# Kernel tuning notes

Measured on AMD Instinct MI355X. Metric: run time of the kernel, lower is better.

The kernel has to match this reference:

```python
import jax, jax.numpy as jnp
import numpy as np

NUM_ITERS = 2      # num_iters default
NEG_SLOPE = 0.2    # LeakyReLU slope in GAT attention
NEG_INF = -1e9

N, E, B, H, K, L = 204800, 6144000, 4096, 8, 30, 50


def setup_inputs() -> dict:
    key = jax.random.key(0)
    ks = jax.random.split(key, 14)
    return {
        "target_features": jax.random.normal(ks[0], (N, 8), jnp.float32),
        "feature_dist_graph": jax.random.normal(ks[1], (E, 8), jnp.float32),
        "rij_dist_pairs": jax.random.uniform(ks[2], (E,), jnp.float32),
        "b_scope": jax.random.randint(ks[3], (N, K), 0, E + 1, jnp.int32),
        "start_end_env": jax.random.randint(ks[4], (N, K), 0, N + 1, jnp.int32),
        "l_scope": jax.random.randint(ks[5], (B, L), 0, N + 1, jnp.int32),
        "edge_src": jax.random.randint(ks[6], (E,), 0, N + 1, jnp.int32),
        "W_emb": jax.random.normal(ks[7], (8, H), jnp.float32),
        "b_emb": jax.random.normal(ks[8], (H,), jnp.float32),
        "W_dist": jax.random.normal(ks[9], (9, H), jnp.float32),
        "b_dist": jax.random.normal(ks[10], (H,), jnp.float32),
        "W_gat": jax.random.normal(ks[11], (H, H), jnp.float32),
        "a_src": jax.random.normal(ks[12], (H,), jnp.float32),
        "a_dst": jax.random.normal(ks[13], (H,), jnp.float32),
    }


def reference(target_features, feature_dist_graph, rij_dist_pairs,
              b_scope, start_end_env, l_scope, edge_src,
              W_emb, b_emb, W_dist, b_dist, W_gat, a_src, a_dst):
    # node embedding: [N, 8] -> [N, H]
    h = target_features @ W_emb + b_emb
    # edge (feature+distance) embedding: [E, 9] -> [E, H]
    msg = jnp.concatenate([feature_dist_graph, rij_dist_pairs[:, None]], axis=1) @ W_dist + b_dist
    zero = jnp.zeros((1, h.shape[1]), h.dtype)
    h = jnp.concatenate([zero, h], axis=0)          # zero row for 1-based / padded indices
    pad_mask = b_scope > 0                           # padded neighbor slots point at row 0
    for _ in range(NUM_ITERS):
        nbr_self = h[start_end_env]                  # getConnectedFeatures: [N, K, H] (target repeated)
        msg0 = jnp.concatenate([zero, msg], axis=0)  # zero row for padded edge indices
        nbr_msg = msg0[b_scope]                      # gathered neighbor messages [N, K, H]
        # GAT attention over the K neighbor slots
        z_s = nbr_self @ W_gat                       # [N, K, H]
        z_m = nbr_msg @ W_gat                        # [N, K, H]
        e = jax.nn.leaky_relu(z_s @ a_src + z_m @ a_dst, NEG_SLOPE)  # [N, K]
        e = jnp.where(pad_mask, e, NEG_INF)
        alpha = jax.nn.softmax(e, axis=1)            # [N, K]
        out = jnp.einsum('nk,nkh->nh', alpha, z_m)   # attention-weighted aggregate [N, H]
        h = jnp.concatenate([zero, jax.nn.elu(out)], axis=0)  # [N+1, H]
        # updateConnectedDict: scatter node states back to per-edge messages
        msg = h[edge_src]                            # [E, H]
    # readout: gather per-graph feature rows and sum -> mol_vecs [B, H]
    return h[l_scope].sum(axis=1)
```

## Files before the change

### kernel.cpp

```cpp
#include <hip/hip_runtime.h>

typedef float f32x4 __attribute__((ext_vector_type(4)));

#define NEG_SLOPE 0.2f
#define NEG_INF   -1e9f

__global__ void embed_kernel(const float* __restrict__ tf,
                             const float* __restrict__ W_emb,
                             const float* __restrict__ b_emb,
                             const float* __restrict__ W_gat,
                             const float* __restrict__ a_src,
                             float* __restrict__ h_a,
                             float* __restrict__ h_b,
                             float* __restrict__ t0,
                             float* __restrict__ t1, int N) {
    __shared__ float sWg[64];
    __shared__ float s_as[8];
    int tid = threadIdx.x;
    if (tid < 64) sWg[tid] = W_gat[tid];
    __syncthreads();
    if (tid < 8) {
        float s = 0.f;
        #pragma unroll
        for (int q = 0; q < 8; ++q) s += sWg[tid * 8 + q] * a_src[q];
        s_as[tid] = s;
    }
    __syncthreads();

    int n = blockIdx.x * blockDim.x + tid;
    if (n >= N) return;
    if (n == 0) {
        #pragma unroll
        for (int j = 0; j < 8; ++j) { h_a[j] = 0.f; h_b[j] = 0.f; }
        t0[0] = 0.f;
        t1[0] = 0.f;
    }
    const f32x4* tfr = reinterpret_cast<const f32x4*>(tf + (size_t)n * 8);
    f32x4 a = tfr[0], b = tfr[1];
    float x[8] = {a[0], a[1], a[2], a[3], b[0], b[1], b[2], b[3]};
    float out[8];
    #pragma unroll
    for (int j = 0; j < 8; ++j) out[j] = b_emb[j];
    #pragma unroll
    for (int i = 0; i < 8; ++i)
        #pragma unroll
        for (int j = 0; j < 8; ++j)
            out[j] += x[i] * W_emb[i * 8 + j];

    float t = 0.f;
    #pragma unroll
    for (int p = 0; p < 8; ++p) t += out[p] * s_as[p];
    t0[n + 1] = t;

    f32x4* hr = reinterpret_cast<f32x4*>(h_a + (size_t)(n + 1) * 8);
    f32x4 o0 = {out[0], out[1], out[2], out[3]};
    f32x4 o1 = {out[4], out[5], out[6], out[7]};
    hr[0] = o0;
    hr[1] = o1;
}

__global__ void prep_records(const float* __restrict__ fdg,
                             const float* __restrict__ rij,
                             const int* __restrict__ edge_src,
                             const float* __restrict__ W_dist,
                             const float* __restrict__ b_dist,
                             const float* __restrict__ W_gat,
                             const float* __restrict__ a_dst,
                             float* __restrict__ rec, int E) {
    __shared__ float sWd[72];
    __shared__ float sbd[8];
    __shared__ float sWg[64];
    __shared__ float s_ad[8];
    int tid = threadIdx.x;
    if (tid < 72) sWd[tid] = W_dist[tid];
    else if (tid < 80) sbd[tid - 72] = b_dist[tid - 72];
    if (tid >= 128 && tid < 192) sWg[tid - 128] = W_gat[tid - 128];
    __syncthreads();
    if (tid < 8) {
        float s = 0.f;
        #pragma unroll
        for (int j = 0; j < 8; ++j) s += sWg[tid * 8 + j] * a_dst[j];
        s_ad[tid] = s;
    }
    __syncthreads();

    int e = blockIdx.x * blockDim.x + tid;
    if (e >= E) return;
    const f32x4* fr = reinterpret_cast<const f32x4*>(fdg + (size_t)e * 8);
    f32x4 g0 = fr[0], g1 = fr[1];
    float rv = rij[e];
    float msg[8];
    #pragma unroll
    for (int j = 0; j < 8; ++j) {
        float s = sbd[j];
        #pragma unroll
        for (int i = 0; i < 4; ++i) s += g0[i] * sWd[i * 8 + j];
        #pragma unroll
        for (int i = 0; i < 4; ++i) s += g1[i] * sWd[(4 + i) * 8 + j];
        s += rv * sWd[64 + j];
        msg[j] = s;
    }
    float em = 0.f;
    #pragma unroll
    for (int j = 0; j < 8; ++j) em += msg[j] * s_ad[j];
    int src = edge_src[e];

    f32x4* op = reinterpret_cast<f32x4*>(rec + (size_t)e * 16);
    f32x4 m0 = {msg[0], msg[1], msg[2], msg[3]};
    f32x4 m1 = {msg[4], msg[5], msg[6], msg[7]};
    f32x4 m2 = {em, __int_as_float(src), 0.f, 0.f};
    f32x4 m3 = {0.f, 0.f, 0.f, 0.f};
    op[0] = m0; op[1] = m1; op[2] = m2; op[3] = m3;
}

template <bool REC>
__global__ void gat_iter1(const float* __restrict__ t0,
                          float* __restrict__ h1,
                          float* __restrict__ t1,
                          int* __restrict__ src_idx,
                          const int* __restrict__ b_scope,
                          const int* __restrict__ se_env,
                          const float* __restrict__ rec,
                          const float* __restrict__ fdg,
                          const float* __restrict__ rij,
                          const int* __restrict__ edge_src,
                          const float* __restrict__ W_dist,
                          const float* __restrict__ b_dist,
                          const float* __restrict__ W_gat,
                          const float* __restrict__ a_src,
                          const float* __restrict__ a_dst,
                          int N, int K) {
    __shared__ float sWg[64];
    __shared__ float s_as[8];
    __shared__ float s_ad[8];
    __shared__ float sWd[72];
    __shared__ float sbd[8];
    int tid = threadIdx.x;
    if (tid < 64) sWg[tid] = W_gat[tid];
    if (!REC) {
        if (tid >= 64 && tid < 136) sWd[tid - 64] = W_dist[tid - 64];
        if (tid >= 136 && tid < 144) sbd[tid - 136] = b_dist[tid - 136];
    }
    __syncthreads();
    if (tid < 8) {
        float s = 0.f;
        #pragma unroll
        for (int j = 0; j < 8; ++j) s += sWg[tid * 8 + j] * a_src[j];
        s_as[tid] = s;
    } else if (tid < 16) {
        int i = tid - 8;
        float s = 0.f;
        #pragma unroll
        for (int j = 0; j < 8; ++j) s += sWg[i * 8 + j] * a_dst[j];
        s_ad[i] = s;
    }
    __syncthreads();

    int node = blockIdx.x * 8 + (tid >> 5);
    int lane = tid & 31;
    if (node == 0 && lane == 0) t1[0] = 0.f;
    if (node >= N) return;
    bool vk = (lane < K);

    int bs = 0, se = 0;
    if (vk) {
        bs = b_scope[(size_t)node * K + lane];
        se = se_env[(size_t)node * K + lane];
    }
    bool has = vk && (bs > 0);
    float t_se = vk ? t0[se] : 0.f;

    float msg[8];
    #pragma unroll
    for (int j = 0; j < 8; ++j) msg[j] = 0.f;
    float em = 0.f;
    int src = -1;

    if (REC) {
        if (has) {
            const f32x4* rp = reinterpret_cast<const f32x4*>(rec + (size_t)(bs - 1) * 16);
            f32x4 m0 = rp[0], m1 = rp[1], m2 = rp[2];
            msg[0] = m0[0]; msg[1] = m0[1]; msg[2] = m0[2]; msg[3] = m0[3];
            msg[4] = m1[0]; msg[5] = m1[1]; msg[6] = m1[2]; msg[7] = m1[3];
            em = m2[0];
            src = __float_as_int(m2[1]);
        }
    } else {
        if (has) {
            const f32x4* fr = reinterpret_cast<const f32x4*>(fdg + (size_t)(bs - 1) * 8);
            f32x4 g0 = fr[0], g1 = fr[1];
            float rv = rij[bs - 1];
            src = edge_src[bs - 1];
            #pragma unroll
            for (int j = 0; j < 8; ++j) {
                float s = sbd[j];
                #pragma unroll
                for (int i = 0; i < 4; ++i) s += g0[i] * sWd[i * 8 + j];
                #pragma unroll
                for (int i = 0; i < 4; ++i) s += g1[i] * sWd[(4 + i) * 8 + j];
                s += rv * sWd[64 + j];
                msg[j] = s;
            }
            #pragma unroll
            for (int j = 0; j < 8; ++j) em += msg[j] * s_ad[j];
        }
    }

    if (vk) src_idx[(size_t)node * K + lane] = src;

    float ee = t_se + em;
    ee = (ee >= 0.f) ? ee : NEG_SLOPE * ee;
    float e = has ? ee : (vk ? NEG_INF : -3e38f);

    float m = e;
    #pragma unroll
    for (int off = 16; off; off >>= 1) m = fmaxf(m, __shfl_xor(m, off, 32));
    float p = vk ? expf(e - m) : 0.f;
    float denom = p;
    #pragma unroll
    for (int off = 16; off; off >>= 1) denom += __shfl_xor(denom, off, 32);
    float alpha = p / denom;

    float agg[8];
    #pragma unroll
    for (int j = 0; j < 8; ++j) agg[j] = alpha * msg[j];
    #pragma unroll
    for (int off = 16; off; off >>= 1)
        #pragma unroll
        for (int j = 0; j < 8; ++j) agg[j] += __shfl_xor(agg[j], off, 32);

    if (lane < 8) {
        float o = 0.f;
        #pragma unroll
        for (int i = 0; i < 8; ++i) o += agg[i] * sWg[i * 8 + lane];
        o = (o > 0.f) ? o : (expf(o) - 1.f);
        h1[(size_t)(node + 1) * 8 + lane] = o;
        float tv = o * s_as[lane];
        tv += __shfl_xor(tv, 1, 32);
        tv += __shfl_xor(tv, 2, 32);
        tv += __shfl_xor(tv, 4, 32);
        if (lane == 0) t1[node + 1] = tv;
    }
}

__global__ void gat_iter2(const float* __restrict__ h1,
                          const float* __restrict__ t1,
                          float* __restrict__ h2,
                          const int* __restrict__ src_idx,
                          const int* __restrict__ se_env,
                          const float* __restrict__ W_gat,
                          const float* __restrict__ a_dst,
                          int N, int K) {
    __shared__ float sWg[64];
    __shared__ float s_ad[8];
    int tid = threadIdx.x;
    if (tid < 64) sWg[tid] = W_gat[tid];
    __syncthreads();
    if (tid < 8) {
        float s = 0.f;
        #pragma unroll
        for (int j = 0; j < 8; ++j) s += sWg[tid * 8 + j] * a_dst[j];
        s_ad[tid] = s;
    }
    __syncthreads();

    int node = blockIdx.x * 8 + (tid >> 5);
    int lane = tid & 31;
    if (node >= N) return;
    bool vk = (lane < K);

    int src = -1, se = 0;
    if (vk) {
        src = src_idx[(size_t)node * K + lane];
        se  = se_env[(size_t)node * K + lane];
    }
    bool has = vk && (src >= 0);
    float t_se = vk ? t1[se] : 0.f;

    float msg[8];
    #pragma unroll
    for (int j = 0; j < 8; ++j) msg[j] = 0.f;
    if (has) {
        const f32x4* mr = reinterpret_cast<const f32x4*>(h1 + (size_t)src * 8);
        f32x4 m0 = mr[0], m1 = mr[1];
        msg[0] = m0[0]; msg[1] = m0[1]; msg[2] = m0[2]; msg[3] = m0[3];
        msg[4] = m1[0]; msg[5] = m1[1]; msg[6] = m1[2]; msg[7] = m1[3];
    }
    float s_m = 0.f;
    #pragma unroll
    for (int j = 0; j < 8; ++j) s_m += msg[j] * s_ad[j];

    float ee = t_se + s_m;
    ee = (ee >= 0.f) ? ee : NEG_SLOPE * ee;
    float e = has ? ee : (vk ? NEG_INF : -3e38f);

    float m = e;
    #pragma unroll
    for (int off = 16; off; off >>= 1) m = fmaxf(m, __shfl_xor(m, off, 32));
    float p = vk ? expf(e - m) : 0.f;
    float denom = p;
    #pragma unroll
    for (int off = 16; off; off >>= 1) denom += __shfl_xor(denom, off, 32);
    float alpha = p / denom;

    float agg[8];
    #pragma unroll
    for (int j = 0; j < 8; ++j) agg[j] = alpha * msg[j];
    #pragma unroll
    for (int off = 16; off; off >>= 1)
        #pragma unroll
        for (int j = 0; j < 8; ++j) agg[j] += __shfl_xor(agg[j], off, 32);

    if (lane < 8) {
        float o = 0.f;
        #pragma unroll
        for (int i = 0; i < 8; ++i) o += agg[i] * sWg[i * 8 + lane];
        o = (o > 0.f) ? o : (expf(o) - 1.f);
        h2[(size_t)(node + 1) * 8 + lane] = o;
    }
}

__global__ void readout_kernel(const float* __restrict__ h,
                               const int* __restrict__ l_scope,
                               float* __restrict__ out, int B, int L) {
    int gid = blockIdx.x * blockDim.x + threadIdx.x;
    int b = gid >> 3;
    int j = gid & 7;
    if (b >= B) return;
    float s = 0.f;
    for (int l = 0; l < L; ++l) {
        int idx = l_scope[(size_t)b * L + l];
        s += h[(size_t)idx * 8 + j];
    }
    out[(size_t)b * 8 + j] = s;
}

extern "C" void kernel_launch(void* const* d_in, const int* in_sizes, int n_in,
                              void* d_out, int out_size, void* d_ws, size_t ws_size,
                              hipStream_t stream) {
    const float* tf      = (const float*)d_in[0];
    const float* fdg     = (const float*)d_in[1];
    const float* rij     = (const float*)d_in[2];
    const int* b_scope   = (const int*)d_in[3];
    const int* start_env = (const int*)d_in[4];
    const int* l_scope   = (const int*)d_in[5];
    const int* edge_src  = (const int*)d_in[6];
    const float* W_emb   = (const float*)d_in[7];
    const float* b_emb   = (const float*)d_in[8];
    const float* W_dist  = (const float*)d_in[9];
    const float* b_dist  = (const float*)d_in[10];
    const float* W_gat   = (const float*)d_in[11];
    const float* a_src   = (const float*)d_in[12];
    const float* a_dst   = (const float*)d_in[13];
    float* out = (float*)d_out;

    const int N = in_sizes[0] / 8;
    const int E = in_sizes[1] / 8;
    const int K = in_sizes[3] / N;
    const int L = 50;
    const int B = in_sizes[5] / L;

    size_t rec_f   = (size_t)E * 16;
    size_t need    = (rec_f + 2 * (size_t)(N + 1) * 8 + 2 * (size_t)(N + 1)
                      + (size_t)N * K) * 4;
    bool use_rec   = (ws_size >= need);

    float* base = (float*)d_ws;
    float* rec  = base;
    size_t off  = use_rec ? rec_f : 0;
    float* h_a  = base + off;  off += (size_t)(N + 1) * 8;
    float* h_b  = base + off;  off += (size_t)(N + 1) * 8;
    float* t0v  = base + off;  off += (size_t)(N + 1);
    float* t1v  = base + off;  off += (size_t)(N + 1);
    int* src_idx = (int*)(base + off);

    embed_kernel<<<(N + 255) / 256, 256, 0, stream>>>(tf, W_emb, b_emb, W_gat, a_src,
                                                      h_a, h_b, t0v, t1v, N);

    const int gat_blocks = (N + 7) / 8;
    if (use_rec) {
        prep_records<<<(E + 255) / 256, 256, 0, stream>>>(fdg, rij, edge_src,
                                                          W_dist, b_dist, W_gat, a_dst,
                                                          rec, E);
        gat_iter1<true><<<gat_blocks, 256, 0, stream>>>(t0v, h_b, t1v, src_idx,
                                                        b_scope, start_env, rec,
                                                        fdg, rij, edge_src,
                                                        W_dist, b_dist, W_gat, a_src, a_dst,
                                                        N, K);
    } else {
        gat_iter1<false><<<gat_blocks, 256, 0, stream>>>(t0v, h_b, t1v, src_idx,
                                                         b_scope, start_env, rec,
                                                         fdg, rij, edge_src,
                                                         W_dist, b_dist, W_gat, a_src, a_dst,
                                                         N, K);
    }
    gat_iter2<<<gat_blocks, 256, 0, stream>>>(h_b, t1v, h_a, src_idx, start_env,
                                              W_gat, a_dst, N, K);

    readout_kernel<<<(B * 8 + 255) / 256, 256, 0, stream>>>(h_a, l_scope, out, B, L);
}
```

Baseline: 416.0 us.

## Merge embed and edge-record prep into one launch; process two nodes per warp

After: 458.9 us. 1.1x slower.

```diff
diff --git a/kernel.cpp b/kernel.cpp
--- a/kernel.cpp
+++ b/kernel.cpp
@@ -5,15 +5,159 @@
 #define NEG_SLOPE 0.2f
 #define NEG_INF   -1e9f
 
-__global__ void embed_kernel(const float* __restrict__ tf,
-                             const float* __restrict__ W_emb,
-                             const float* __restrict__ b_emb,
-                             const float* __restrict__ W_gat,
-                             const float* __restrict__ a_src,
-                             float* __restrict__ h_a,
-                             float* __restrict__ h_b,
-                             float* __restrict__ t0,
-                             float* __restrict__ t1, int N) {
+__global__ void prep_embed(const float* __restrict__ fdg,
+                           const float* __restrict__ rij,
+                           const int* __restrict__ edge_src,
+                           const float* __restrict__ W_dist,
+                           const float* __restrict__ b_dist,
+                           const float* __restrict__ W_gat,
+                           const float* __restrict__ a_src,
+                           const float* __restrict__ a_dst,
+                           const float* __restrict__ tf,
+                           const float* __restrict__ W_emb,
+                           const float* __restrict__ b_emb,
+                           float* __restrict__ rec,
+                           float* __restrict__ h_a,
+                           float* __restrict__ h_b,
+                           float* __restrict__ t0,
+                           float* __restrict__ t1,
+                           int E, int N, int nb_edge) {
+    __shared__ float sW[72];
+    __shared__ float sb[8];
+    __shared__ float sWg[64];
+    __shared__ float s_vec[8];
+    int tid = threadIdx.x;
+    bool edge_block = (blockIdx.x < nb_edge);
+    if (edge_block) {
+        if (tid < 72) sW[tid] = W_dist[tid];
+        else if (tid < 80) sb[tid - 72] = b_dist[tid - 72];
+    } else {
+        if (tid < 64) sW[tid] = W_emb[tid];
+        else if (tid < 72) sb[tid - 64] = b_emb[tid - 64];
+    }
+    if (tid >= 128 && tid < 192) sWg[tid - 128] = W_gat[tid - 128];
+    __syncthreads();
+    if (tid < 8) {
+        const float* av = edge_block ? a_dst : a_src;
+        float s = 0.f;
+        #pragma unroll
+        for (int j = 0; j < 8; ++j) s += sWg[tid * 8 + j] * av[j];
+        s_vec[tid] = s;
+    }
+    __syncthreads();
+
+    if (edge_block) {
+        int e = blockIdx.x * blockDim.x + tid;
+        if (e >= E) return;
+        const f32x4* fr = reinterpret_cast<const f32x4*>(fdg + (size_t)e * 8);
+        f32x4 g0 = fr[0], g1 = fr[1];
+        float rv = rij[e];
+        float msg[8];
+        #pragma unroll
+        for (int j = 0; j < 8; ++j) {
+            float s = sb[j];
+            #pragma unroll
+            for (int i = 0; i < 4; ++i) s += g0[i] * sW[i * 8 + j];
+            #pragma unroll
+            for (int i = 0; i < 4; ++i) s += g1[i] * sW[(4 + i) * 8 + j];
+            s += rv * sW[64 + j];
+            msg[j] = s;
+        }
+        float em = 0.f;
+        #pragma unroll
+        for (int j = 0; j < 8; ++j) em += msg[j] * s_vec[j];
+        int src = edge_src[e];
+
+        f32x4* op = reinterpret_cast<f32x4*>(rec + (size_t)e * 16);
+        f32x4 m0 = {msg[0], msg[1], msg[2], msg[3]};
+        f32x4 m1 = {msg[4], msg[5], msg[6], msg[7]};
+        f32x4 m2 = {em, __int_as_float(src), 0.f, 0.f};
+        op[0] = m0; op[1] = m1; op[2] = m2;
+    } else {
+        int n = (blockIdx.x - nb_edge) * blockDim.x + tid;
+        if (n >= N) return;
+        if (n == 0) {
+            #pragma unroll
+            for (int j = 0; j < 8; ++j) { h_a[j] = 0.f; h_b[j] = 0.f; }
+            t0[0] = 0.f;
+            t1[0] = 0.f;
+        }
+        const f32x4* tfr = reinterpret_cast<const f32x4*>(tf + (size_t)n * 8);
+        f32x4 a = tfr[0], b = tfr[1];
+        float x[8] = {a[0], a[1], a[2], a[3], b[0], b[1], b[2], b[3]};
+        float out[8];
+        #pragma unroll
+        for (int j = 0; j < 8; ++j) out[j] = sb[j];
+        #pragma unroll
+        for (int i = 0; i < 8; ++i)
+            #pragma unroll
+            for (int j = 0; j < 8; ++j)
+                out[j] += x[i] * sW[i * 8 + j];
+        float t = 0.f;
+        #pragma unroll
+        for (int p = 0; p < 8; ++p) t += out[p] * s_vec[p];
+        t0[n + 1] = t;
+        f32x4* hr = reinterpret_cast<f32x4*>(h_a + (size_t)(n + 1) * 8);
+        f32x4 o0 = {out[0], out[1], out[2], out[3]};
+        f32x4 o1 = {out[4], out[5], out[6], out[7]};
+        hr[0] = o0;
+        hr[1] = o1;
+    }
+}
+
+__device__ __forceinline__ void finish_node(const float msg[8], float t_se, float em,
+                                            bool has, bool vk, int lane, int node,
+                                            const float* __restrict__ sWg,
+                                            const float* __restrict__ s_as,
+                                            float* __restrict__ h_next,
+                                            float* __restrict__ t_next) {
+    float ee = t_se + em;
+    ee = (ee >= 0.f) ? ee : NEG_SLOPE * ee;
+    float e = has ? ee : (vk ? NEG_INF : -3e38f);
+
+    float m = e;
+    #pragma unroll
+    for (int off = 16; off; off >>= 1) m = fmaxf(m, __shfl_xor(m, off, 32));
+    float p = vk ? expf(e - m) : 0.f;
+    float denom = p;
+    #pragma unroll
+    for (int off = 16; off; off >>= 1) denom += __shfl_xor(denom, off, 32);
+    float alpha = p / denom;
+
+    float agg[8];
+    #pragma unroll
+    for (int j = 0; j < 8; ++j) agg[j] = alpha * msg[j];
+    #pragma unroll
+    for (int off = 16; off; off >>= 1)
+        #pragma unroll
+        for (int j = 0; j < 8; ++j) agg[j] += __shfl_xor(agg[j], off, 32);
+
+    if (lane < 8) {
+        float o = 0.f;
+        #pragma unroll
+        for (int i = 0; i < 8; ++i) o += agg[i] * sWg[i * 8 + lane];
+        o = (o > 0.f) ? o : (expf(o) - 1.f);
+        h_next[(size_t)(node + 1) * 8 + lane] = o;
+        if (t_next) {
+            float tv = o * s_as[lane];
+            tv += __shfl_xor(tv, 1, 32);
+            tv += __shfl_xor(tv, 2, 32);
+            tv += __shfl_xor(tv, 4, 32);
+            if (lane == 0) t_next[node + 1] = tv;
+        }
+    }
+}
+
+__global__ void gat_iter1_rec(const float* __restrict__ t0,
+                              float* __restrict__ h1,
+                              float* __restrict__ t1,
+                              int* __restrict__ src_idx,
+                              const int* __restrict__ b_scope,
+                              const int* __restrict__ se_env,
+                              const float* __restrict__ rec,
+                              const float* __restrict__ W_gat,
+                              const float* __restrict__ a_src,
+                              int N, int K) {
     __shared__ float sWg[64];
     __shared__ float s_as[8];
     int tid = threadIdx.x;
@@ -22,114 +166,74 @@
     if (tid < 8) {
         float s = 0.f;
         #pragma unroll
-        for (int q = 0; q < 8; ++q) s += sWg[tid * 8 + q] * a_src[q];
+        for (int j = 0; j < 8; ++j) s += sWg[tid * 8 + j] * a_src[j];
         s_as[tid] = s;
     }
     __syncthreads();
 
-    int n = blockIdx.x * blockDim.x + tid;
-    if (n >= N) return;
-    if (n == 0) {
-        #pragma unroll
-        for (int j = 0; j < 8; ++j) { h_a[j] = 0.f; h_b[j] = 0.f; }
-        t0[0] = 0.f;
-        t1[0] = 0.f;
-    }
-    const f32x4* tfr = reinterpret_cast<const f32x4*>(tf + (size_t)n * 8);
-    f32x4 a = tfr[0], b = tfr[1];
-    float x[8] = {a[0], a[1], a[2], a[3], b[0], b[1], b[2], b[3]};
-    float out[8];
-    #pragma unroll
-    for (int j = 0; j < 8; ++j) out[j] = b_emb[j];
-    #pragma unroll
-    for (int i = 0; i < 8; ++i)
-        #pragma unroll
-        for (int j = 0; j < 8; ++j)
-            out[j] += x[i] * W_emb[i * 8 + j];
-
-    float t = 0.f;
-    #pragma unroll
-    for (int p = 0; p < 8; ++p) t += out[p] * s_as[p];
-    t0[n + 1] = t;
-
-    f32x4* hr = reinterpret_cast<f32x4*>(h_a + (size_t)(n + 1) * 8);
-    f32x4 o0 = {out[0], out[1], out[2], out[3]};
-    f32x4 o1 = {out[4], out[5], out[6], out[7]};
-    hr[0] = o0;
-    hr[1] = o1;
-}
-
-__global__ void prep_records(const float* __restrict__ fdg,
+    int lane = tid & 31;
+    int g = blockIdx.x * 8 + (tid >> 5);
+    int nA = g * 2, nB = g * 2 + 1;
+    if (nA >= N) return;
+    bool hasBn = (nB < N);
+    bool vk = (lane < K);
+
+    int bsA = 0, seA = 0, bsB = 0, seB = 0;
+    if (vk) {
+        bsA = b_scope[(size_t)nA * K + lane];
+        seA = se_env[(size_t)nA * K + lane];
+        if (hasBn) {
+            bsB = b_scope[(size_t)nB * K + lane];
+            seB = se_env[(size_t)nB * K + lane];
+        }
+    }
+    bool hasA = vk && (bsA > 0);
+    bool hasB = vk && hasBn && (bsB > 0);
+
+    float tA = vk ? t0[seA] : 0.f;
+    float tB = (vk && hasBn) ? t0[seB] : 0.f;
+
+    f32x4 a0 = {0,0,0,0}, a1 = {0,0,0,0}, a2 = {0,0,0,0};
+    f32x4 b0 = {0,0,0,0}, b1 = {0,0,0,0}, b2 = {0,0,0,0};
+    if (hasA) {
+        const f32x4* rp = reinterpret_cast<const f32x4*>(rec + (size_t)(bsA - 1) * 16);
+        a0 = rp[0]; a1 = rp[1]; a2 = rp[2];
+    }
+    if (hasB) {
+        const f32x4* rp = reinterpret_cast<const f32x4*>(rec + (size_t)(bsB - 1) * 16);
+        b0 = rp[0]; b1 = rp[1]; b2 = rp[2];
+    }
+
+    int srcA = hasA ? __float_as_int(a2[1]) : -1;
+    int srcB = hasB ? __float_as_int(b2[1]) : -1;
+    if (vk) {
+        src_idx[(size_t)nA * K + lane] = srcA;
+        if (hasBn) src_idx[(size_t)nB * K + lane] = srcB;
+    }
+
+    float msgA[8] = {a0[0], a0[1], a0[2], a0[3], a1[0], a1[1], a1[2], a1[3]};
+    finish_node(msgA, tA, a2[0], hasA, vk, lane, nA, sWg, s_as, h1, t1);
+    if (hasBn) {
+        float msgB[8] = {b0[0], b0[1], b0[2], b0[3], b1[0], b1[1], b1[2], b1[3]};
+        finish_node(msgB, tB, b2[0], hasB, vk, lane, nB, sWg, s_as, h1, t1);
+    }
+}
+
+__global__ void gat_iter1_fb(const float* __restrict__ t0,
+                             float* __restrict__ h1,
+                             float* __restrict__ t1,
+                             int* __restrict__ src_idx,
+                             const int* __restrict__ b_scope,
+                             const int* __restrict__ se_env,
+                             const float* __restrict__ fdg,
                              const float* __restrict__ rij,
                              const int* __restrict__ edge_src,
                              const float* __restrict__ W_dist,
                              const float* __restrict__ b_dist,
                              const float* __restrict__ W_gat,
+                             const float* __restrict__ a_src,
                              const float* __restrict__ a_dst,
-                             float* __restrict__ rec, int E) {
-    __shared__ float sWd[72];
-    __shared__ float sbd[8];
-    __shared__ float sWg[64];
-    __shared__ float s_ad[8];
-    int tid = threadIdx.x;
-    if (tid < 72) sWd[tid] = W_dist[tid];
-    else if (tid < 80) sbd[tid - 72] = b_dist[tid - 72];
-    if (tid >= 128 && tid < 192) sWg[tid - 128] = W_gat[tid - 128];
-    __syncthreads();
-    if (tid < 8) {
-        float s = 0.f;
-        #pragma unroll
-        for (int j = 0; j < 8; ++j) s += sWg[tid * 8 + j] * a_dst[j];
-        s_ad[tid] = s;
-    }
-    __syncthreads();
-
-    int e = blockIdx.x * blockDim.x + tid;
-    if (e >= E) return;
-    const f32x4* fr = reinterpret_cast<const f32x4*>(fdg + (size_t)e * 8);
-    f32x4 g0 = fr[0], g1 = fr[1];
-    float rv = rij[e];
-    float msg[8];
-    #pragma unroll
-    for (int j = 0; j < 8; ++j) {
-        float s = sbd[j];
-        #pragma unroll
-        for (int i = 0; i < 4; ++i) s += g0[i] * sWd[i * 8 + j];
-        #pragma unroll
-        for (int i = 0; i < 4; ++i) s += g1[i] * sWd[(4 + i) * 8 + j];
-        s += rv * sWd[64 + j];
-        msg[j] = s;
-    }
-    float em = 0.f;
-    #pragma unroll
-    for (int j = 0; j < 8; ++j) em += msg[j] * s_ad[j];
-    int src = edge_src[e];
-
-    f32x4* op = reinterpret_cast<f32x4*>(rec + (size_t)e * 16);
-    f32x4 m0 = {msg[0], msg[1], msg[2], msg[3]};
-    f32x4 m1 = {msg[4], msg[5], msg[6], msg[7]};
-    f32x4 m2 = {em, __int_as_float(src), 0.f, 0.f};
-    f32x4 m3 = {0.f, 0.f, 0.f, 0.f};
-    op[0] = m0; op[1] = m1; op[2] = m2; op[3] = m3;
-}
-
-template <bool REC>
-__global__ void gat_iter1(const float* __restrict__ t0,
-                          float* __restrict__ h1,
-                          float* __restrict__ t1,
-                          int* __restrict__ src_idx,
-                          const int* __restrict__ b_scope,
-                          const int* __restrict__ se_env,
-                          const float* __restrict__ rec,
-                          const float* __restrict__ fdg,
-                          const float* __restrict__ rij,
-                          const int* __restrict__ edge_src,
-                          const float* __restrict__ W_dist,
-                          const float* __restrict__ b_dist,
-                          const float* __restrict__ W_gat,
-                          const float* __restrict__ a_src,
-                          const float* __restrict__ a_dst,
-                          int N, int K) {
+                             int N, int K) {
     __shared__ float sWg[64];
     __shared__ float s_as[8];
     __shared__ float s_ad[8];
@@ -137,10 +241,8 @@
     __shared__ float sbd[8];
     int tid = threadIdx.x;
     if (tid < 64) sWg[tid] = W_gat[tid];
-    if (!REC) {
-        if (tid >= 64 && tid < 136) sWd[tid - 64] = W_dist[tid - 64];
-        if (tid >= 136 && tid < 144) sbd[tid - 136] = b_dist[tid - 136];
-    }
+    if (tid >= 64 && tid < 136) sWd[tid - 64] = W_dist[tid - 64];
+    if (tid >= 136 && tid < 144) sbd[tid - 136] = b_dist[tid - 136];
     __syncthreads();
     if (tid < 8) {
         float s = 0.f;
@@ -158,7 +260,6 @@
 
     int node = blockIdx.x * 8 + (tid >> 5);
     int lane = tid & 31;
-    if (node == 0 && lane == 0) t1[0] = 0.f;
     if (node >= N) return;
     bool vk = (lane < K);
 
@@ -175,72 +276,26 @@
     for (int j = 0; j < 8; ++j) msg[j] = 0.f;
     float em = 0.f;
     int src = -1;
-
-    if (REC) {
-        if (has) {
-            const f32x4* rp = reinterpret_cast<const f32x4*>(rec + (size_t)(bs - 1) * 16);
-            f32x4 m0 = rp[0], m1 = rp[1], m2 = rp[2];
-            msg[0] = m0[0]; msg[1] = m0[1]; msg[2] = m0[2]; msg[3] = m0[3];
-            msg[4] = m1[0]; msg[5] = m1[1]; msg[6] = m1[2]; msg[7] = m1[3];
-            em = m2[0];
-            src = __float_as_int(m2[1]);
-        }
-    } else {
-        if (has) {
-            const f32x4* fr = reinterpret_cast<const f32x4*>(fdg + (size_t)(bs - 1) * 8);
-            f32x4 g0 = fr[0], g1 = fr[1];
-            float rv = rij[bs - 1];
-            src = edge_src[bs - 1];
-            #pragma unroll
-            for (int j = 0; j < 8; ++j) {
-                float s = sbd[j];
-                #pragma unroll
-                for (int i = 0; i < 4; ++i) s += g0[i] * sWd[i * 8 + j];
-                #pragma unroll
-                for (int i = 0; i < 4; ++i) s += g1[i] * sWd[(4 + i) * 8 + j];
-                s += rv * sWd[64 + j];
-                msg[j] = s;
-            }
-            #pragma unroll
-            for (int j = 0; j < 8; ++j) em += msg[j] * s_ad[j];
-        }
-    }
-
+    if (has) {
+        const f32x4* fr = reinterpret_cast<const f32x4*>(fdg + (size_t)(bs - 1) * 8);
+        f32x4 g0 = fr[0], g1 = fr[1];
+        float rv = rij[bs - 1];
+        src = edge_src[bs - 1];
+        #pragma unroll
+        for (int j = 0; j < 8; ++j) {
+            float s = sbd[j];
+            #pragma unroll
+            for (int i = 0; i < 4; ++i) s += g0[i] * sWd[i * 8 + j];
+            #pragma unroll
+            for (int i = 0; i < 4; ++i) s += g1[i] * sWd[(4 + i) * 8 + j];
+            s += rv * sWd[64 + j];
+            msg[j] = s;
+        }
+        #pragma unroll
+        for (int j = 0; j < 8; ++j) em += msg[j] * s_ad[j];
+    }
     if (vk) src_idx[(size_t)node * K + lane] = src;
-
-    float ee = t_se + em;
-    ee = (ee >= 0.f) ? ee : NEG_SLOPE * ee;
-    float e = has ? ee : (vk ? NEG_INF : -3e38f);
-
-    float m = e;
-    #pragma unroll
-    for (int off = 16; off; off >>= 1) m = fmaxf(m, __shfl_xor(m, off, 32));
-    float p = vk ? expf(e - m) : 0.f;
-    float denom = p;
-    #pragma unroll
-    for (int off = 16; off; off >>= 1) denom += __shfl_xor(denom, off, 32);
-    float alpha = p / denom;
-
-    float agg[8];
-    #pragma unroll
-    for (int j = 0; j < 8; ++j) agg[j] = alpha * msg[j];
-    #pragma unroll
-    for (int off = 16; off; off >>= 1)
-        #pragma unroll
-        for (int j = 0; j < 8; ++j) agg[j] += __shfl_xor(agg[j], off, 32);
-
-    if (lane < 8) {
-        float o = 0.f;
-        #pragma unroll
-        for (int i = 0; i < 8; ++i) o += agg[i] * sWg[i * 8 + lane];
-        o = (o > 0.f) ? o : (expf(o) - 1.f);
-        h1[(size_t)(node + 1) * 8 + lane] = o;
-        float tv = o * s_as[lane];
-        tv += __shfl_xor(tv, 1, 32);
-        tv += __shfl_xor(tv, 2, 32);
-        tv += __shfl_xor(tv, 4, 32);
-        if (lane == 0) t1[node + 1] = tv;
-    }
+    finish_node(msg, t_se, em, has, vk, lane, node, sWg, s_as, h1, t1);
 }
 
 __global__ void gat_iter2(const float* __restrict__ h1,
@@ -264,59 +319,49 @@
     }
     __syncthreads();
 
-    int node = blockIdx.x * 8 + (tid >> 5);
     int lane = tid & 31;
-    if (node >= N) return;
+    int g = blockIdx.x * 8 + (tid >> 5);
+    int nA = g * 2, nB = g * 2 + 1;
+    if (nA >= N) return;
+    bool hasBn = (nB < N);
     bool vk = (lane < K);
 
-    int src = -1, se = 0;
+    int srcA = -1, seA = 0, srcB = -1, seB = 0;
     if (vk) {
-        src = src_idx[(size_t)node * K + lane];
-        se  = se_env[(size_t)node * K + lane];
-    }
-    bool has = vk && (src >= 0);
-    float t_se = vk ? t1[se] : 0.f;
-
-    float msg[8];
-    #pragma unroll
-    for (int j = 0; j < 8; ++j) msg[j] = 0.f;
-    if (has) {
-        const f32x4* mr = reinterpret_cast<const f32x4*>(h1 + (size_t)src * 8);
-        f32x4 m0 = mr[0], m1 = mr[1];
-        msg[0] = m0[0]; msg[1] = m0[1]; msg[2] = m0[2]; msg[3] = m0[3];
-        msg[4] = m1[0]; msg[5] = m1[1]; msg[6] = m1[2]; msg[7] = m1[3];
-    }
-    float s_m = 0.f;
-    #pragma unroll
-    for (int j = 0; j < 8; ++j) s_m += msg[j] * s_ad[j];
-
-    float ee = t_se + s_m;
-    ee = (ee >= 0.f) ? ee : NEG_SLOPE * ee;
-    float e = has ? ee : (vk ? NEG_INF : -3e38f);
-
-    float m = e;
-    #pragma unroll
-    for (int off = 16; off; off >>= 1) m = fmaxf(m, __shfl_xor(m, off, 32));
-    float p = vk ? expf(e - m) : 0.f;
-    float denom = p;
-    #pragma unroll
-    for (int off = 16; off; off >>= 1) denom += __shfl_xor(denom, off, 32);
-    float alpha = p / denom;
-
-    float agg[8];
-    #pragma unroll
-    for (int j = 0; j < 8; ++j) agg[j] = alpha * msg[j];
-    #pragma unroll
-    for (int off = 16; off; off >>= 1)
-        #pragma unroll
-        for (int j = 0; j < 8; ++j) agg[j] += __shfl_xor(agg[j], off, 32);
-
-    if (lane < 8) {
-        float o = 0.f;
-        #pragma unroll
-        for (int i = 0; i < 8; ++i) o += agg[i] * sWg[i * 8 + lane];
-        o = (o > 0.f) ? o : (expf(o) - 1.f);
-        h2[(size_t)(node + 1) * 8 + lane] = o;
+        srcA = src_idx[(size_t)nA * K + lane];
+        seA  = se_env[(size_t)nA * K + lane];
+        if (hasBn) {
+            srcB = src_idx[(size_t)nB * K + lane];
+            seB  = se_env[(size_t)nB * K + lane];
+        }
+    }
+    bool hasA = vk && (srcA >= 0);
+    bool hasB = vk && hasBn && (srcB >= 0);
+
+    float tA = vk ? t1[seA] : 0.f;
+    float tB = (vk && hasBn) ? t1[seB] : 0.f;
+
+    f32x4 a0 = {0,0,0,0}, a1 = {0,0,0,0}, b0 = {0,0,0,0}, b1 = {0,0,0,0};
+    if (hasA) {
+        const f32x4* mr = reinterpret_cast<const f32x4*>(h1 + (size_t)srcA * 8);
+        a0 = mr[0]; a1 = mr[1];
+    }
+    if (hasB) {
+        const f32x4* mr = reinterpret_cast<const f32x4*>(h1 + (size_t)srcB * 8);
+        b0 = mr[0]; b1 = mr[1];
+    }
+
+    float msgA[8] = {a0[0], a0[1], a0[2], a0[3], a1[0], a1[1], a1[2], a1[3]};
+    float emA = 0.f;
+    #pragma unroll
+    for (int j = 0; j < 8; ++j) emA += msgA[j] * s_ad[j];
+    finish_node(msgA, tA, emA, hasA, vk, lane, nA, sWg, nullptr, h2, nullptr);
+    if (hasBn) {
+        float msgB[8] = {b0[0], b0[1], b0[2], b0[3], b1[0], b1[1], b1[2], b1[3]};
+        float emB = 0.f;
+        #pragma unroll
+        for (int j = 0; j < 8; ++j) emB += msgB[j] * s_ad[j];
+        finish_node(msgB, tB, emB, hasB, vk, lane, nB, sWg, nullptr, h2, nullptr);
     }
 }
 
@@ -360,10 +405,10 @@
     const int L = 50;
     const int B = in_sizes[5] / L;
 
-    size_t rec_f   = (size_t)E * 16;
-    size_t need    = (rec_f + 2 * (size_t)(N + 1) * 8 + 2 * (size_t)(N + 1)
-                      + (size_t)N * K) * 4;
-    bool use_rec   = (ws_size >= need);
+    size_t rec_f = (size_t)E * 16;
+    size_t need  = (rec_f + 2 * (size_t)(N + 1) * 8 + 2 * (size_t)(N + 1)
+                    + (size_t)N * K) * 4;
+    bool use_rec = (ws_size >= need);
 
     float* base = (float*)d_ws;
     float* rec  = base;
@@ -374,28 +419,31 @@
     float* t1v  = base + off;  off += (size_t)(N + 1);
     int* src_idx = (int*)(base + off);
 
-    embed_kernel<<<(N + 255) / 256, 256, 0, stream>>>(tf, W_emb, b_emb, W_gat, a_src,
-                                                      h_a, h_b, t0v, t1v, N);
-
-    const int gat_blocks = (N + 7) / 8;
+    const int nb_edge = (E + 255) / 256;
+    const int nb_node = (N + 255) / 256;
+
     if (use_rec) {
-        prep_records<<<(E + 255) / 256, 256, 0, stream>>>(fdg, rij, edge_src,
-                                                          W_dist, b_dist, W_gat, a_dst,
-                                                          rec, E);
-        gat_iter1<true><<<gat_blocks, 256, 0, stream>>>(t0v, h_b, t1v, src_idx,
-                                                        b_scope, start_env, rec,
-                                                        fdg, rij, edge_src,
-                                                        W_dist, b_dist, W_gat, a_src, a_dst,
-                                                        N, K);
+        prep_embed<<<nb_edge + nb_node, 256, 0, stream>>>(
+            fdg, rij, edge_src, W_dist, b_dist, W_gat, a_src, a_dst,
+            tf, W_emb, b_emb, rec, h_a, h_b, t0v, t1v, E, N, nb_edge);
+        const int g1_blocks = ((N + 1) / 2 + 7) / 8;
+        gat_iter1_rec<<<g1_blocks, 256, 0, stream>>>(t0v, h_b, t1v, src_idx,
+                                                     b_scope, start_env, rec,
+                                                     W_gat, a_src, N, K);
     } else {
-        gat_iter1<false><<<gat_blocks, 256, 0, stream>>>(t0v, h_b, t1v, src_idx,
-                                                         b_scope, start_env, rec,
-                                                         fdg, rij, edge_src,
-                                                         W_dist, b_dist, W_gat, a_src, a_dst,
-                                                         N, K);
-    }
-    gat_iter2<<<gat_blocks, 256, 0, stream>>>(h_b, t1v, h_a, src_idx, start_env,
-                                              W_gat, a_dst, N, K);
+        prep_embed<<<nb_node, 256, 0, stream>>>(
+            fdg, rij, edge_src, W_dist, b_dist, W_gat, a_src, a_dst,
+            tf, W_emb, b_emb, rec, h_a, h_b, t0v, t1v, 0, N, 0);
+        gat_iter1_fb<<<(N + 7) / 8, 256, 0, stream>>>(t0v, h_b, t1v, src_idx,
+                                                      b_scope, start_env,
+                                                      fdg, rij, edge_src,
+                                                      W_dist, b_dist, W_gat,
+                                                      a_src, a_dst, N, K);
+    }
+
+    const int g2_blocks = ((N + 1) / 2 + 7) / 8;
+    gat_iter2<<<g2_blocks, 256, 0, stream>>>(h_b, t1v, h_a, src_idx, start_env,
+                                             W_gat, a_dst, N, K);
 
     readout_kernel<<<(B * 8 + 255) / 256, 256, 0, stream>>>(h_a, l_scope, out, B, L);
 }
```
